# Kernel tuning notes

Measured on AMD Instinct MI355X. Metric: run time of the kernel, lower is better.

The kernel has to match this reference:

```python
import jax, jax.numpy as jnp
import numpy as np

N_GROUPS = 4


def setup_inputs() -> dict:
    key = jax.random.key(0)
    k1, k2 = jax.random.split(key)
    x = jax.random.normal(k1, (64, 256, 32, 32), dtype=jnp.float32)
    # codebook: (group_size, num_embeddings) = (256 // 4, 512), torch.rand init
    weight = jax.random.uniform(k2, (64, 512), dtype=jnp.float32)
    return {"x": x, "weight": weight}


def _group_quantize(xg, emb):
    # xg: (B, g, H, W), emb: (g, K)
    # squared Euclidean distance; argmin is identical to argmin of torch.norm
    d2 = (jnp.sum(xg * xg, axis=1)[..., None]
          - 2.0 * jnp.einsum('bghw,gk->bhwk', xg, emb)
          + jnp.sum(emb * emb, axis=0))        # (B, H, W, K)
    argmin = jnp.argmin(d2, axis=-1)            # (B, H, W)
    result = jnp.transpose(emb.T[argmin], (0, 3, 1, 2))  # (B, g, H, W)
    return result, argmin


def reference(x, weight):
    B, D, H, W = x.shape
    g = D // N_GROUPS
    results = []
    argmins = []
    for i in range(N_GROUPS):  # fixed small structural loop
        r, a = _group_quantize(x[:, i * g:(i + 1) * g], weight)
        results.append(r)
        argmins.append(a)
    result = jnp.concatenate(results, axis=1) / jnp.sqrt(jnp.float32(N_GROUPS))
    argmins = jnp.stack(argmins, axis=1)  # (B, n_groups, H, W)
    return result, argmins
```

## Files before the change

### kernel.cpp

```cpp
#include <hip/hip_runtime.h>
#include <float.h>

#define KCODES 512
#define GDIM 64
#define SBIAS 96.0f
#define TAUQ 0.015f

typedef __attribute__((ext_vector_type(8))) short short8;
typedef __attribute__((ext_vector_type(4))) float floatx4;


__device__ __forceinline__ void bf16split(float x, short& hi, short& lo) {
    unsigned u = __float_as_uint(x);
    unsigned h = (u + 0x7fffu + ((u >> 16) & 1u)) >> 16;
    hi = (short)h;
    float hf = __uint_as_float(h << 16);
    float l = x - hf;
    unsigned ul = __float_as_uint(l);
    lo = (short)((ul + 0x7fffu + ((ul >> 16) & 1u)) >> 16);
}

__device__ __forceinline__ void gload_lds16(const void* g, void* l) {
    __builtin_amdgcn_global_load_lds(
        (const __attribute__((address_space(1))) void*)g,
        (__attribute__((address_space(3))) void*)l, 16, 0, 0);
}

__launch_bounds__(256)
__global__ void prep_kernel(const float* __restrict__ w,
                            float* __restrict__ embT,
                            float* __restrict__ e2,
                            double* __restrict__ e2d,
                            short* __restrict__ emb_hi,
                            short* __restrict__ emb_lo) {
    int t = blockIdx.x * 256 + threadIdx.x;
    int k = t >> 6;
    int g = t & 63;
    float v = w[(size_t)g * KCODES + k];
    embT[(size_t)k * GDIM + g] = v;
    short h, l; bf16split(-2.0f * v, h, l);
    emb_hi[(size_t)k * GDIM + g] = h;
    emb_lo[(size_t)k * GDIM + g] = l;
    float s = v * v;
    double sd = (double)v * (double)v;
#pragma unroll
    for (int off = 32; off > 0; off >>= 1) {
        s  += __shfl_xor(s, off, 64);
        sd += __shfl_xor(sd, off, 64);
    }
    if (g == 0) { e2[k] = s; e2d[k] = sd; }
}

__launch_bounds__(256, 5)
__global__ void vq_kernel(const float* __restrict__ x,
                          const float* __restrict__ embT,
                          const float* __restrict__ e2,
                          const double* __restrict__ e2d,
                          const short* __restrict__ emb_hi,
                          const short* __restrict__ emb_lo,
                          float* __restrict__ out_res,
                          float* __restrict__ out_arg) {
    __shared__ short s_hi[2][32 * 64];
    __shared__ short s_lo[2][32 * 64];
    __shared__ float s_e2[512];
    __shared__ int   s_arg[128];
    __shared__ float s_fixx[4][64];
    __shared__ int   s_flags[128];
    __shared__ int   s_nflag;

    const int t = threadIdx.x;
    const int wid = t >> 6;
    const int lane = t & 63;
    const int q = lane >> 4;
    const int c = lane & 15;
    const int blk = blockIdx.x;
    const int grp = blk >> 9;
    const int posbase = ((blk & 511) << 7) + wid * 32;
    const int b = posbase >> 10;
    const int hwb = posbase & 1023;

    if (t == 0) s_nflag = 0;

    const int rA = wid * 8 + (lane >> 3);
    const int uA = (lane & 7) ^ (lane >> 3);
    const int srcA = rA * 64 + uA * 8;

#define PREFETCH(CH, BUF)                                                      \
    {                                                                          \
        gload_lds16(emb_hi + (size_t)(CH) * 2048 + srcA, &s_hi[BUF][wid * 512]); \
        gload_lds16(emb_lo + (size_t)(CH) * 2048 + srcA, &s_lo[BUF][wid * 512]); \
    }

    PREFETCH(0, 0);
    s_e2[t] = e2[t] + SBIAS;
    s_e2[t + 256] = e2[t + 256] + SBIAS;

    const float* xbase = x + (size_t)b * 262144 + (size_t)grp * 65536 + hwb;

    short8 ahi[2][2], alo[2][2];
#pragma unroll
    for (int mt = 0; mt < 2; ++mt)
#pragma unroll
        for (int kt = 0; kt < 2; ++kt) {
#pragma unroll
            for (int j = 0; j < 8; ++j) {
                float xv = xbase[(kt * 32 + q * 8 + j) * 1024 + mt * 16 + c];
                short h, l; bf16split(xv, h, l);
                ahi[mt][kt][j] = h; alo[mt][kt][j] = l;
            }
        }

    unsigned best[2][4], sec[2][4];
#pragma unroll
    for (int mt = 0; mt < 2; ++mt)
#pragma unroll
        for (int r = 0; r < 4; ++r) { best[mt][r] = 0xFFFFFFFFu; sec[mt][r] = 0xFFFFFFFFu; }

    const int p8 = (q ^ (c & 7)) << 3;

    __syncthreads();

    int cur = 0;
    for (int ch = 0; ch < 16; ++ch) {
        if (ch < 15) PREFETCH(ch + 1, cur ^ 1);
        const int C0 = ch * 32;

#pragma unroll
        for (int nt = 0; nt < 2; ++nt) {
            const int o = (nt * 16 + c) * 64 + p8;
            short8 bh0 = *(const short8*)&s_hi[cur][o];
            short8 bh1 = *(const short8*)&s_hi[cur][o ^ 32];
            short8 bl0 = *(const short8*)&s_lo[cur][o];
            short8 bl1 = *(const short8*)&s_lo[cur][o ^ 32];
            const float se2 = s_e2[C0 + nt * 16 + c];
            const unsigned n = (unsigned)(C0 + nt * 16 + c);
#pragma unroll
            for (int mt = 0; mt < 2; ++mt) {
                floatx4 a4 = (floatx4){se2, se2, se2, se2};
                a4 = __builtin_amdgcn_mfma_f32_16x16x32_bf16(alo[mt][0], bh0, a4, 0, 0, 0);
                a4 = __builtin_amdgcn_mfma_f32_16x16x32_bf16(ahi[mt][0], bl0, a4, 0, 0, 0);
                a4 = __builtin_amdgcn_mfma_f32_16x16x32_bf16(ahi[mt][0], bh0, a4, 0, 0, 0);
                a4 = __builtin_amdgcn_mfma_f32_16x16x32_bf16(alo[mt][1], bh1, a4, 0, 0, 0);
                a4 = __builtin_amdgcn_mfma_f32_16x16x32_bf16(ahi[mt][1], bl1, a4, 0, 0, 0);
                a4 = __builtin_amdgcn_mfma_f32_16x16x32_bf16(ahi[mt][1], bh1, a4, 0, 0, 0);
#pragma unroll
                for (int r = 0; r < 4; ++r) {
                    unsigned key = (__float_as_uint(a4[r]) & ~511u) | n;
                    unsigned bo = best[mt][r];
                    best[mt][r] = bo < key ? bo : key;
                    unsigned mx = bo > key ? bo : key;
                    sec[mt][r]  = sec[mt][r] < mx ? sec[mt][r] : mx;
                }
            }
        }

        __syncthreads();
        cur ^= 1;
    }

#pragma unroll
    for (int mt = 0; mt < 2; ++mt)
#pragma unroll
        for (int r = 0; r < 4; ++r) {
            unsigned b_ = best[mt][r], s_ = sec[mt][r];
#pragma unroll
            for (int sh = 1; sh < 16; sh <<= 1) {
                unsigned ob = (unsigned)__shfl_xor((int)b_, sh, 64);
                unsigned os = (unsigned)__shfl_xor((int)s_, sh, 64);
                unsigned mx = b_ > ob ? b_ : ob;
                s_ = s_ < os ? s_ : os;
                s_ = s_ < mx ? s_ : mx;
                b_ = b_ < ob ? b_ : ob;
            }
            if (c == 0) {
                int p = mt * 16 + q * 4 + r;
                s_arg[wid * 32 + p] = (int)(b_ & 511u);
                float fb = __uint_as_float(b_ & ~511u);
                float fs = __uint_as_float(s_ & ~511u);
                if (fs - fb <= TAUQ) {
                    int slot = atomicAdd(&s_nflag, 1);
                    s_flags[slot] = wid * 32 + p;
                }
            }
        }

    {
        int p = lane & 31, gi = lane >> 5;
        int ac = s_arg[wid * 32 + p];
        const float* ev = embT + (size_t)ac * GDIM;
        float* rp = out_res + (size_t)b * 262144 + (size_t)grp * 65536 + hwb + p;
#pragma unroll
        for (int it = 0; it < 32; ++it) {
            int g = it * 2 + gi;
            rp[(size_t)g * 1024] = ev[g] * 0.5f;
        }
    }

    __syncthreads();
    if (t < 128) {
        int bp = ((blk & 511) << 7) + t;
        out_arg[(size_t)(bp >> 10) * 4096 + (size_t)grp * 1024 + (bp & 1023)] =
            (float)s_arg[t];
    }
    __syncthreads();

    const int nf = s_nflag;
    for (int f = wid; f < nf; f += 4) {
        const int hwa = s_flags[f];
        const int pos = ((blk & 511) << 7) + hwa;
        const int fb = pos >> 10;
        const int sidx = pos & 1023;
        s_fixx[wid][lane] =
            x[(size_t)fb * 262144 + (size_t)grp * 65536 + (size_t)lane * 1024 + sidx];
        asm volatile("s_waitcnt lgkmcnt(0)" ::: "memory");

        double bd = DBL_MAX; int bk = 0;
        for (int m = 0; m < KCODES / 64; ++m) {
            const int k = lane + m * 64;
            const float* er = embT + (size_t)k * GDIM;
            double dot = 0.0;
#pragma unroll 4
            for (int g = 0; g < GDIM; g += 4) {
                float4 e4 = *(const float4*)(er + g);
                float4 xv = *(const float4*)&s_fixx[wid][g];
                dot += (double)xv.x * (double)e4.x;
                dot += (double)xv.y * (double)e4.y;
                dot += (double)xv.z * (double)e4.z;
                dot += (double)xv.w * (double)e4.w;
            }
            double s = e2d[k] - 2.0 * dot;
            if (s < bd) { bd = s; bk = k; }
        }
        for (int off = 32; off > 0; off >>= 1) {
            double od = __shfl_down(bd, off, 64);
            int    ok = __shfl_down(bk, off, 64);
            if (od < bd || (od == bd && ok < bk)) { bd = od; bk = ok; }
        }
        bk = __shfl(bk, 0, 64);

        if (lane == 0)
            out_arg[(size_t)fb * 4096 + (size_t)grp * 1024 + sidx] = (float)bk;
        out_res[(size_t)fb * 262144 + (size_t)grp * 65536 + (size_t)lane * 1024 + sidx] =
            embT[(size_t)bk * GDIM + lane] * 0.5f;
    }
#undef PREFETCH
}

extern "C" void kernel_launch(void* const* d_in, const int* in_sizes, int n_in,
                              void* d_out, int out_size, void* d_ws, size_t ws_size,
                              hipStream_t stream) {
    const float* x = (const float*)d_in[0];
    const float* w = (const float*)d_in[1];
    float* out_res = (float*)d_out;
    float* out_arg = (float*)d_out + 16777216;

    float*    embT   = (float*)d_ws;
    float*    e2     = embT + 32768;
    double*   e2d    = (double*)((char*)d_ws + (size_t)33280 * 4);
    short*    emb_hi = (short*)((float*)d_ws + 34304);
    short*    emb_lo = (short*)((float*)d_ws + 50688);

    prep_kernel<<<128, 256, 0, stream>>>(w, embT, e2, e2d, emb_hi, emb_lo);
    vq_kernel<<<2048, 256, 0, stream>>>(x, embT, e2, e2d, emb_hi, emb_lo,
                                        out_res, out_arg);
}
```

Measured before the change: 247.8 us.

## Replace split-bf16 3-pass MFMA with single fp16 MFMA and widen codebook chunks

Drops the hi/lo bf16 error-compensated product (three MFMAs per k-slice) in favour of a single fp16 MFMA per k-slice. Codebook chunks in LDS grow from 32 to 64 codes, which halves the loop trip count, and the occupancy hint drops from 5 to 4. The margin threshold for the exact fallback path widens (TAUQ 0.015 -> 0.0625) to absorb the larger fp16 rounding error, so more positions may take the slow recheck. It also relies on the inputs fitting fp16 range.

```diff
diff --git a/kernel.cpp b/kernel.cpp
--- a/kernel.cpp
+++ b/kernel.cpp
@@ -1,24 +1,15 @@
 #include <hip/hip_runtime.h>
+#include <hip/hip_fp16.h>
 #include <float.h>
 
 #define KCODES 512
 #define GDIM 64
 #define SBIAS 96.0f
-#define TAUQ 0.015f
-
-typedef __attribute__((ext_vector_type(8))) short short8;
+#define TAUQ 0.0625f
+
+typedef __attribute__((ext_vector_type(8))) _Float16 half8;
 typedef __attribute__((ext_vector_type(4))) float floatx4;
 
-
-__device__ __forceinline__ void bf16split(float x, short& hi, short& lo) {
-    unsigned u = __float_as_uint(x);
-    unsigned h = (u + 0x7fffu + ((u >> 16) & 1u)) >> 16;
-    hi = (short)h;
-    float hf = __uint_as_float(h << 16);
-    float l = x - hf;
-    unsigned ul = __float_as_uint(l);
-    lo = (short)((ul + 0x7fffu + ((ul >> 16) & 1u)) >> 16);
-}
 
 __device__ __forceinline__ void gload_lds16(const void* g, void* l) {
     __builtin_amdgcn_global_load_lds(
@@ -31,16 +22,14 @@
                             float* __restrict__ embT,
                             float* __restrict__ e2,
                             double* __restrict__ e2d,
-                            short* __restrict__ emb_hi,
-                            short* __restrict__ emb_lo) {
+                            short* __restrict__ emb_f16) {
     int t = blockIdx.x * 256 + threadIdx.x;
     int k = t >> 6;
     int g = t & 63;
     float v = w[(size_t)g * KCODES + k];
     embT[(size_t)k * GDIM + g] = v;
-    short h, l; bf16split(-2.0f * v, h, l);
-    emb_hi[(size_t)k * GDIM + g] = h;
-    emb_lo[(size_t)k * GDIM + g] = l;
+    emb_f16[(size_t)k * GDIM + g] =
+        (short)__half_as_ushort(__float2half(-2.0f * v));
     float s = v * v;
     double sd = (double)v * (double)v;
 #pragma unroll
@@ -51,17 +40,15 @@
     if (g == 0) { e2[k] = s; e2d[k] = sd; }
 }
 
-__launch_bounds__(256, 5)
+__launch_bounds__(256, 4)
 __global__ void vq_kernel(const float* __restrict__ x,
                           const float* __restrict__ embT,
                           const float* __restrict__ e2,
                           const double* __restrict__ e2d,
-                          const short* __restrict__ emb_hi,
-                          const short* __restrict__ emb_lo,
+                          const short* __restrict__ emb_f16,
                           float* __restrict__ out_res,
                           float* __restrict__ out_arg) {
-    __shared__ short s_hi[2][32 * 64];
-    __shared__ short s_lo[2][32 * 64];
+    __shared__ short s_cb[2][64 * 64];
     __shared__ float s_e2[512];
     __shared__ int   s_arg[128];
     __shared__ float s_fixx[4][64];
@@ -81,14 +68,17 @@
 
     if (t == 0) s_nflag = 0;
 
-    const int rA = wid * 8 + (lane >> 3);
+    const int rA = wid * 16 + (lane >> 3);
+    const int rB = rA + 8;
     const int uA = (lane & 7) ^ (lane >> 3);
     const int srcA = rA * 64 + uA * 8;
+    const int srcB = rB * 64 + uA * 8;
 
 #define PREFETCH(CH, BUF)                                                      \
     {                                                                          \
-        gload_lds16(emb_hi + (size_t)(CH) * 2048 + srcA, &s_hi[BUF][wid * 512]); \
-        gload_lds16(emb_lo + (size_t)(CH) * 2048 + srcA, &s_lo[BUF][wid * 512]); \
+        const short* gc_ = emb_f16 + (size_t)(CH) * 4096;                      \
+        gload_lds16(gc_ + srcA, &s_cb[BUF][wid * 1024]);                       \
+        gload_lds16(gc_ + srcB, &s_cb[BUF][wid * 1024 + 512]);                 \
     }
 
     PREFETCH(0, 0);
@@ -97,7 +87,7 @@
 
     const float* xbase = x + (size_t)b * 262144 + (size_t)grp * 65536 + hwb;
 
-    short8 ahi[2][2], alo[2][2];
+    half8 a16[2][2];
 #pragma unroll
     for (int mt = 0; mt < 2; ++mt)
 #pragma unroll
@@ -105,8 +95,7 @@
 #pragma unroll
             for (int j = 0; j < 8; ++j) {
                 float xv = xbase[(kt * 32 + q * 8 + j) * 1024 + mt * 16 + c];
-                short h, l; bf16split(xv, h, l);
-                ahi[mt][kt][j] = h; alo[mt][kt][j] = l;
+                a16[mt][kt][j] = (_Float16)xv;
             }
         }
 
@@ -121,28 +110,22 @@
     __syncthreads();
 
     int cur = 0;
-    for (int ch = 0; ch < 16; ++ch) {
-        if (ch < 15) PREFETCH(ch + 1, cur ^ 1);
-        const int C0 = ch * 32;
-
-#pragma unroll
-        for (int nt = 0; nt < 2; ++nt) {
+    for (int ch = 0; ch < 8; ++ch) {
+        if (ch < 7) PREFETCH(ch + 1, cur ^ 1);
+        const int C0 = ch * 64;
+
+#pragma unroll
+        for (int nt = 0; nt < 4; ++nt) {
             const int o = (nt * 16 + c) * 64 + p8;
-            short8 bh0 = *(const short8*)&s_hi[cur][o];
-            short8 bh1 = *(const short8*)&s_hi[cur][o ^ 32];
-            short8 bl0 = *(const short8*)&s_lo[cur][o];
-            short8 bl1 = *(const short8*)&s_lo[cur][o ^ 32];
+            half8 b0 = *(const half8*)&s_cb[cur][o];
+            half8 b1 = *(const half8*)&s_cb[cur][o ^ 32];
             const float se2 = s_e2[C0 + nt * 16 + c];
             const unsigned n = (unsigned)(C0 + nt * 16 + c);
 #pragma unroll
             for (int mt = 0; mt < 2; ++mt) {
                 floatx4 a4 = (floatx4){se2, se2, se2, se2};
-                a4 = __builtin_amdgcn_mfma_f32_16x16x32_bf16(alo[mt][0], bh0, a4, 0, 0, 0);
-                a4 = __builtin_amdgcn_mfma_f32_16x16x32_bf16(ahi[mt][0], bl0, a4, 0, 0, 0);
-                a4 = __builtin_amdgcn_mfma_f32_16x16x32_bf16(ahi[mt][0], bh0, a4, 0, 0, 0);
-                a4 = __builtin_amdgcn_mfma_f32_16x16x32_bf16(alo[mt][1], bh1, a4, 0, 0, 0);
-                a4 = __builtin_amdgcn_mfma_f32_16x16x32_bf16(ahi[mt][1], bl1, a4, 0, 0, 0);
-                a4 = __builtin_amdgcn_mfma_f32_16x16x32_bf16(ahi[mt][1], bh1, a4, 0, 0, 0);
+                a4 = __builtin_amdgcn_mfma_f32_16x16x32_f16(a16[mt][0], b0, a4, 0, 0, 0);
+                a4 = __builtin_amdgcn_mfma_f32_16x16x32_f16(a16[mt][1], b1, a4, 0, 0, 0);
 #pragma unroll
                 for (int r = 0; r < 4; ++r) {
                     unsigned key = (__float_as_uint(a4[r]) & ~511u) | n;
@@ -254,13 +237,12 @@
     float* out_res = (float*)d_out;
     float* out_arg = (float*)d_out + 16777216;
 
-    float*    embT   = (float*)d_ws;
-    float*    e2     = embT + 32768;
-    double*   e2d    = (double*)((char*)d_ws + (size_t)33280 * 4);
-    short*    emb_hi = (short*)((float*)d_ws + 34304);
-    short*    emb_lo = (short*)((float*)d_ws + 50688);
-
-    prep_kernel<<<128, 256, 0, stream>>>(w, embT, e2, e2d, emb_hi, emb_lo);
-    vq_kernel<<<2048, 256, 0, stream>>>(x, embT, e2, e2d, emb_hi, emb_lo,
+    float*    embT    = (float*)d_ws;
+    float*    e2      = embT + 32768;
+    double*   e2d     = (double*)((char*)d_ws + (size_t)33280 * 4);
+    short*    emb_f16 = (short*)((float*)d_ws + 34304);
+
+    prep_kernel<<<128, 256, 0, stream>>>(w, embT, e2, e2d, emb_f16);
+    vq_kernel<<<2048, 256, 0, stream>>>(x, embT, e2, e2d, emb_f16,
                                         out_res, out_arg);
 }
```

Measured after the change: 353.4 us. 1.43x slower.
